# Optimization experiments

Measured on AMD Instinct MI355X. Metric: run time of the kernel, lower is better.

## Reference

```python
import jax, jax.numpy as jnp
import numpy as np

NUM_CLASSES = 81
THRESHOLD = 0.5
NEGPOS_RATIO = 3
VARIANCE = (0.1, 0.2)
B, P, O = 32, 24564, 50


def point_form(pr):
    # center-form (cx,cy,w,h) -> corner-form (x1,y1,x2,y2)
    return jnp.concatenate([pr[:, :2] - pr[:, 2:] / 2, pr[:, :2] + pr[:, 2:] / 2], axis=1)


def jaccard(a, b):
    # a: [O,4] corner-form truths, b: [P,4] corner-form priors -> [O,P]
    lt = jnp.maximum(a[:, None, :2], b[None, :, :2])
    rb = jnp.minimum(a[:, None, 2:], b[None, :, 2:])
    wh = jnp.clip(rb - lt, 0.0)
    inter = wh[..., 0] * wh[..., 1]
    area_a = ((a[:, 2] - a[:, 0]) * (a[:, 3] - a[:, 1]))[:, None]
    area_b = ((b[:, 2] - b[:, 0]) * (b[:, 3] - b[:, 1]))[None, :]
    return inter / (area_a + area_b - inter)


def encode(matched, priors_cf):
    # matched: [P,4] corner-form gt; priors_cf: [P,4] center-form
    g_cxcy = ((matched[:, :2] + matched[:, 2:]) / 2 - priors_cf[:, :2]) / (VARIANCE[0] * priors_cf[:, 2:])
    g_wh = jnp.log((matched[:, 2:] - matched[:, :2]) / priors_cf[:, 2:]) / VARIANCE[1]
    return jnp.concatenate([g_cxcy, g_wh], axis=1)


def match_one(truths, labels, priors_cf, priors_pf):
    ov = jaccard(truths, priors_pf)                       # [O,P]
    best_prior_idx = jnp.argmax(ov, axis=1)               # [O] best prior per truth
    best_truth_overlap = jnp.max(ov, axis=0)              # [P]
    best_truth_idx = jnp.argmax(ov, axis=0)               # [P]
    # ensure every gt matches its best prior
    best_truth_overlap = best_truth_overlap.at[best_prior_idx].set(2.0)
    best_truth_idx = best_truth_idx.at[best_prior_idx].set(jnp.arange(truths.shape[0]))
    matches = truths[best_truth_idx]                      # [P,4]
    conf = labels[best_truth_idx] + 1                     # background = 0
    conf = jnp.where(best_truth_overlap < THRESHOLD, 0, conf)
    loc = encode(matches, priors_cf)
    return loc, conf


def setup_inputs() -> dict:
    key = jax.random.key(0)
    k1, k2, k3, k4, k5, k6, k7 = jax.random.split(key, 7)
    loc_data = jax.random.normal(k1, (B, P, 4), jnp.float32)
    conf_data = jax.random.normal(k2, (B, P, NUM_CLASSES), jnp.float32)
    cxcy = jax.random.uniform(k3, (P, 2), minval=0.05, maxval=0.95)
    wh = jax.random.uniform(k4, (P, 2), minval=0.05, maxval=0.5)
    priors = jnp.concatenate([cxcy, wh], axis=1).astype(jnp.float32)
    gc = jax.random.uniform(k5, (B, O, 2), minval=0.1, maxval=0.9)
    gwh = jax.random.uniform(k6, (B, O, 2), minval=0.05, maxval=0.4)
    boxes = jnp.clip(jnp.concatenate([gc - gwh / 2, gc + gwh / 2], axis=-1), 0.0, 1.0)
    labels = jax.random.randint(k7, (B, O), 0, NUM_CLASSES - 1).astype(jnp.float32)
    targets = jnp.concatenate([boxes, labels[..., None]], axis=-1).astype(jnp.float32)
    return {"loc_data": loc_data, "conf_data": conf_data, "priors": priors, "targets": targets}


def reference(loc_data, conf_data, priors, targets):
    truths = targets[..., :4]                              # [B,O,4]
    labels = targets[..., 4].astype(jnp.int32)             # [B,O]
    priors_pf = point_form(priors)
    loc_t, conf_t = jax.vmap(match_one, in_axes=(0, 0, None, None))(truths, labels, priors, priors_pf)
    pos = conf_t > 0                                       # [B,P]

    # localization smooth-L1 over positives (sum reduction)
    diff = loc_data - loc_t
    sl1 = jnp.where(jnp.abs(diff) < 1.0, 0.5 * diff * diff, jnp.abs(diff) - 0.5)
    loss_l = jnp.sum(sl1 * pos[..., None].astype(sl1.dtype))

    # per-anchor CE loss for hard negative mining
    lse = jax.nn.logsumexp(conf_data, axis=-1)             # [B,P]
    gathered = jnp.take_along_axis(conf_data, conf_t[..., None], axis=-1)[..., 0]
    loss_c_all = lse - gathered                            # [B,P]
    loss_c_mine = jnp.where(pos, 0.0, loss_c_all)
    loss_idx = jnp.argsort(-loss_c_mine, axis=1)
    idx_rank = jnp.argsort(loss_idx, axis=1)
    num_pos = jnp.sum(pos.astype(jnp.int32), axis=1, keepdims=True)  # [B,1]
    num_neg = jnp.minimum(NEGPOS_RATIO * num_pos, P - 1)
    neg = idx_rank < num_neg                               # [B,P]

    sel = jnp.logical_or(pos, neg)
    loss_c = jnp.sum(jnp.where(sel, loss_c_all, 0.0))

    N = jnp.sum(num_pos).astype(loss_l.dtype)
    return loss_l / N, loss_c / N
```

## Files before the change

kernel.cpp:

```cpp
#include <hip/hip_runtime.h>

#define NB 32
#define NP 24564
#define NO 50
#define NC 81
#define THR 0.5f

__device__ __forceinline__ float rl_f(float v, int j) {
  return __uint_as_float((unsigned)__builtin_amdgcn_readlane((int)__float_as_uint(v), j));
}
__device__ __forceinline__ float bp_f(float v, int j4) {
  return __uint_as_float((unsigned)__builtin_amdgcn_ds_bpermute(j4, (int)__float_as_uint(v)));
}


__global__ __launch_bounds__(256) void k0(
    double* __restrict__ acc, int* __restrict__ num_pos,
    float* __restrict__ accLb, float* __restrict__ accCb,
    int* __restrict__ done, unsigned long long* __restrict__ bp) {
  const int tid = threadIdx.x;
  if (tid < 4) acc[tid] = 0.0;
  if (tid < NB) { num_pos[tid] = 0; accLb[tid] = 0.0f; accCb[tid] = 0.0f; }
  if (tid == 4) *done = 0;
  for (int i = tid; i < NB * NO; i += 256) bp[i] = 0ull;
}

#define KA_CHUNK 1024

__global__ __launch_bounds__(256) void kA(
    const float* __restrict__ priors, const float* __restrict__ targets,
    unsigned long long* __restrict__ bp_packed) {
  __shared__ float4 s_pf[KA_CHUNK];
  __shared__ float s_t[NO * 5];
  const int b = blockIdx.y;
  const int tid = threadIdx.x;
  const int base = blockIdx.x * KA_CHUNK;

  for (int i = tid; i < NO * 5; i += 256) s_t[i] = targets[b * NO * 5 + i];

  #pragma unroll
  for (int k = 0; k < KA_CHUNK / 256; ++k) {
    const int p = base + k * 256 + tid;
    float4 pf;
    if (p < NP) {
      const float4 pr = ((const float4*)priors)[p];
      pf = make_float4(pr.x - pr.z * 0.5f, pr.y - pr.w * 0.5f,
                       pr.x + pr.z * 0.5f, pr.y + pr.w * 0.5f);
    } else {
      pf = make_float4(3.0f, 3.0f, 3.0f, 3.0f);
    }
    s_pf[k * 256 + tid] = pf;
  }
  __syncthreads();

  const int wv = tid >> 6;
  const int lane = tid & 63;
  if (lane < NO) {
    const float tx1 = s_t[lane * 5 + 0], ty1 = s_t[lane * 5 + 1];
    const float tx2 = s_t[lane * 5 + 2], ty2 = s_t[lane * 5 + 3];
    const float area_a = (tx2 - tx1) * (ty2 - ty1);
    const int i0 = wv * (KA_CHUNK / 4);
    unsigned long long best = 0ull;
    #pragma unroll 8
    for (int i = 0; i < KA_CHUNK / 4; ++i) {
      const float4 q = s_pf[i0 + i];
      const float ltx = fmaxf(tx1, q.x), lty = fmaxf(ty1, q.y);
      const float rbx = fminf(tx2, q.z), rby = fminf(ty2, q.w);
      const float wx = fmaxf(rbx - ltx, 0.0f), wy = fmaxf(rby - lty, 0.0f);
      const float inter = wx * wy;
      const float ab = (q.z - q.x) * (q.w - q.y);
      const float iou = __fdividef(inter, area_a + ab - inter);
      const unsigned p = (unsigned)(base + i0 + i);
      const unsigned long long pk =
          (((unsigned long long)__float_as_uint(iou)) << 32) |
          (unsigned long long)(0xFFFFFFFFu - p);
      if (pk > best) best = pk;
    }
    atomicMax(&bp_packed[b * NO + lane], best);
  }
}

__global__ __launch_bounds__(256) void kMS(
    const float* __restrict__ loc, const float* __restrict__ conf,
    const float* __restrict__ priors, const float* __restrict__ targets,
    const unsigned* __restrict__ bp32,
    float* __restrict__ mine, int* __restrict__ num_pos,
    float* __restrict__ accLb, float* __restrict__ accCb) {
  __shared__ float s_s[256];
  __shared__ float sLw[4], sCw[4];
  __shared__ int sNw[4];
  const int tid = threadIdx.x;
  const int lane = tid & 63;
  const int b = blockIdx.y;
  const int rowbase = blockIdx.x * 256 + (tid & 192);
  const int p = rowbase + lane;
  const bool valid = (p < NP);
  const int pc = valid ? p : NP - 1;
  const size_t grow = (size_t)b * NP + pc;
  const float* tb = targets + (size_t)b * (NO * 5);

  float ttx1 = 3.f, tty1 = 3.f, ttx2 = 3.f, tty2 = 3.f, tar = 0.f, tlab = 0.f;
  int tpb = -1;
  if (lane < NO) {
    ttx1 = tb[lane * 5 + 0]; tty1 = tb[lane * 5 + 1];
    ttx2 = tb[lane * 5 + 2]; tty2 = tb[lane * 5 + 3];
    tlab = tb[lane * 5 + 4];
    tar = (ttx2 - ttx1) * (tty2 - tty1);
    tpb = (int)(0xFFFFFFFFu - bp32[(b * NO + lane) * 2]);
  }

  const float4 pr = ((const float4*)priors)[pc];
  const float4 ldv = ((const float4*)loc)[grow];
  const float px1 = pr.x - pr.z * 0.5f, py1 = pr.y - pr.w * 0.5f;
  const float px2 = pr.x + pr.z * 0.5f, py2 = pr.y + pr.w * 0.5f;
  const float areab = (px2 - px1) * (py2 - py1);

  float bv = -1.0f;
  int bj = 0;
  #pragma unroll 2
  for (int j = 0; j < NO; ++j) {
    const float x1 = rl_f(ttx1, j), y1 = rl_f(tty1, j);
    const float x2 = rl_f(ttx2, j), y2 = rl_f(tty2, j);
    const float aa = rl_f(tar, j);
    const float wx = fmaxf(fminf(x2, px2) - fmaxf(x1, px1), 0.0f);
    const float wy = fmaxf(fminf(y2, py2) - fmaxf(y1, py1), 0.0f);
    const float inter = wx * wy;
    const float iou = __fdividef(inter, aa + areab - inter);
    if (iou > bv) { bv = iou; bj = j; }
  }

  int ovj = -1;
  unsigned long long M = __ballot((lane < NO) && ((unsigned)(tpb - rowbase) < 64u));
  while (M) {
    const int l = __ffsll((long long)M) - 1;
    M &= M - 1;
    const int r = __builtin_amdgcn_readlane(tpb, l) - rowbase;
    if (lane == r) ovj = l;
  }
  const int jm = (ovj >= 0) ? ovj : bj;
  const bool pos = valid && ((ovj >= 0) || (bv >= THR));
  const int j4 = jm << 2;
  const float lab = bp_f(tlab, j4);
  const float mx1 = bp_f(ttx1, j4), my1 = bp_f(tty1, j4);
  const float mx2 = bp_f(ttx2, j4), my2 = bp_f(tty2, j4);
  const int conft = pos ? ((int)lab + 1) : 0;

  const float gval = conf[grow * NC + conft];

  float sl1 = 0.0f;
  if (pos) {
    const float gcx = __fdividef((mx1 + mx2) * 0.5f - pr.x, 0.1f * pr.z);
    const float gcy = __fdividef((my1 + my2) * 0.5f - pr.y, 0.1f * pr.w);
    const float gw = __logf(__fdividef(mx2 - mx1, pr.z)) * 5.0f;
    const float gh = __logf(__fdividef(my2 - my1, pr.w)) * 5.0f;
    const float d0 = ldv.x - gcx, d1 = ldv.y - gcy;
    const float d2 = ldv.z - gw, d3 = ldv.w - gh;
    #pragma unroll
    for (int q = 0; q < 4; ++q) {
      const float d = (q == 0) ? d0 : (q == 1) ? d1 : (q == 2) ? d2 : d3;
      const float a = fabsf(d);
      sl1 += (a < 1.0f) ? 0.5f * d * d : a - 0.5f;
    }
  }

  const int l16 = lane & 15;
  const int g4 = (lane >> 4) & 3;
  #pragma unroll 2
  for (int ph = 0; ph < 16; ++ph) {
    const int ro = ph * 4 + g4;
    const int rr = rowbase + ro;
    const int rc = (rr < NP) ? rr : NP - 1;
    const float* rowp = conf + ((size_t)b * NP + rc) * NC;
    float s0 = __expf(rowp[l16]);
    float s1 = __expf(rowp[l16 + 16]);
    s0 += __expf(rowp[l16 + 32]);
    s1 += __expf(rowp[l16 + 48]);
    s0 += __expf(rowp[l16 + 64]);
    if (l16 == 0) s1 += __expf(rowp[80]);
    float s = s0 + s1;
    s += __shfl_xor(s, 1, 64);
    s += __shfl_xor(s, 2, 64);
    s += __shfl_xor(s, 4, 64);
    s += __shfl_xor(s, 8, 64);
    if (l16 == 0) s_s[(tid & 192) + ro] = s;
  }
  const float myS = s_s[tid];

  const float lca = __logf(myS) - gval;
  float sumL = 0.0f, sumC = 0.0f;
  int cnt = 0;
  if (valid) {
    mine[grow] = pos ? 0.0f : fmaxf(lca, 0.0f);
    if (pos) { cnt = 1; sumC = lca; sumL = sl1; }
  }

  #pragma unroll
  for (int m = 1; m <= 32; m <<= 1) {
    sumL += __shfl_xor(sumL, m, 64);
    sumC += __shfl_xor(sumC, m, 64);
    cnt  += __shfl_xor(cnt, m, 64);
  }
  const int w = tid >> 6;
  if (lane == 0) { sLw[w] = sumL; sCw[w] = sumC; sNw[w] = cnt; }
  __syncthreads();
  if (tid == 0) {
    const float L = sLw[0] + sLw[1] + sLw[2] + sLw[3];
    const float C = sCw[0] + sCw[1] + sCw[2] + sCw[3];
    const int n = sNw[0] + sNw[1] + sNw[2] + sNw[3];
    if (L != 0.0f) atomicAdd(&accLb[b], L);
    if (C != 0.0f) atomicAdd(&accCb[b], C);
    if (n) atomicAdd(&num_pos[b], n);
  }
}

__global__ __launch_bounds__(512) void kD(
    const float* __restrict__ mine, const int* __restrict__ num_pos,
    double* __restrict__ acc, int* __restrict__ done,
    const float* __restrict__ accLb, const float* __restrict__ accCb,
    float* __restrict__ out) {
  const int b = blockIdx.x;
  const int tid = threadIdx.x;
  const float* vb = mine + (size_t)b * NP;

  unsigned vals[48];
  #pragma unroll
  for (int k = 0; k < 48; ++k) {
    const int i = tid + k * 512;
    vals[k] = (i < NP) ? __float_as_uint(vb[i]) : 0u;
  }

  const int K = min(3 * num_pos[b], NP - 1);

  __shared__ int s_w[2][8];
  unsigned prefix = 0u;
  int remaining = K;

  for (int bit = 30; bit >= 0; --bit) {
    const unsigned want = (prefix >> bit) | 1u;
    int cnt = 0;
    #pragma unroll
    for (int k = 0; k < 48; ++k) cnt += ((vals[k] >> bit) == want) ? 1 : 0;
    #pragma unroll
    for (int m = 32; m >= 1; m >>= 1) cnt += __shfl_xor(cnt, m, 64);
    const int buf = bit & 1;
    if ((tid & 63) == 0) s_w[buf][tid >> 6] = cnt;
    __syncthreads();
    int total = 0;
    #pragma unroll
    for (int w = 0; w < 8; ++w) total += s_w[buf][w];
    if (total >= remaining) prefix |= (1u << bit);
    else remaining -= total;
  }

  if (K > 0) {
    const float t = __uint_as_float(prefix);
    double sg = 0.0;
    int cg = 0;
    #pragma unroll
    for (int k = 0; k < 48; ++k) {
      const float f = __uint_as_float(vals[k]);
      if (f > t) { sg += (double)f; cg++; }
    }
    #pragma unroll
    for (int m = 32; m >= 1; m >>= 1) {
      sg += __shfl_xor(sg, m, 64);
      cg += __shfl_xor(cg, m, 64);
    }
    __shared__ double s_sd[8];
    __shared__ int s_sc[8];
    const int wid = tid >> 6;
    if ((tid & 63) == 0) { s_sd[wid] = sg; s_sc[wid] = cg; }
    __syncthreads();
    if (tid == 0) {
      double S = 0.0;
      int C = 0;
      for (int w = 0; w < 8; ++w) { S += s_sd[w]; C += s_sc[w]; }
      S += (double)(K - C) * (double)t;
      atomicAdd(&acc[2], S);
    }
  }

  __shared__ int s_last;
  __syncthreads();
  if (tid == 0) {
    __threadfence();
    s_last = (atomicAdd(done, 1) == NB - 1) ? 1 : 0;
  }
  __syncthreads();
  if (s_last && tid < 64) {
    int n = 0;
    float L = 0.0f, C = 0.0f;
    if (tid < NB) { n = num_pos[tid]; L = accLb[tid]; C = accCb[tid]; }
    #pragma unroll
    for (int m = 32; m >= 1; m >>= 1) {
      n += __shfl_xor(n, m, 64);
      L += __shfl_xor(L, m, 64);
      C += __shfl_xor(C, m, 64);
    }
    if (tid == 0) {
      const double S = atomicAdd(&acc[2], 0.0);
      const double Nf = (double)n;
      out[0] = (float)((double)L / Nf);
      out[1] = (float)(((double)C + S) / Nf);
    }
  }
}

extern "C" void kernel_launch(void* const* d_in, const int* in_sizes, int n_in,
                              void* d_out, int out_size, void* d_ws, size_t ws_size,
                              hipStream_t stream) {
  const float* loc     = (const float*)d_in[0];
  const float* conf    = (const float*)d_in[1];
  const float* priors  = (const float*)d_in[2];
  const float* targets = (const float*)d_in[3];
  float* out = (float*)d_out;

  char* ws = (char*)d_ws;
  double* acc   = (double*)ws;
  int* num_pos  = (int*)(ws + 32);
  float* accLb  = (float*)(ws + 160);
  float* accCb  = (float*)(ws + 288);
  int* done     = (int*)(ws + 416);
  unsigned long long* bp = (unsigned long long*)(ws + 424);
  const size_t hdr = 13224;
  float* mine  = (float*)(ws + hdr);

  k0<<<1, 256, 0, stream>>>(acc, num_pos, accLb, accCb, done, bp);

  dim3 gA((NP + KA_CHUNK - 1) / KA_CHUNK, NB);
  kA<<<gA, 256, 0, stream>>>(priors, targets, bp);

  dim3 gM((NP + 255) / 256, NB);
  kMS<<<gM, 256, 0, stream>>>(loc, conf, priors, targets, (const unsigned*)bp,
                              mine, num_pos, accLb, accCb);

  kD<<<NB, 512, 0, stream>>>(mine, num_pos, acc, done, accLb, accCb, out);
}
```

Measured before the change: 159.2 us.

## Drop init kernel and atomics via per-chunk best-prior partials; vectorize conf row loads

```diff
diff --git a/kernel.cpp b/kernel.cpp
--- a/kernel.cpp
+++ b/kernel.cpp
@@ -5,6 +5,8 @@
 #define NO 50
 #define NC 81
 #define THR 0.5f
+#define KA_CHUNK 1024
+#define NCH 24
 
 __device__ __forceinline__ float rl_f(float v, int j) {
   return __uint_as_float((unsigned)__builtin_amdgcn_readlane((int)__float_as_uint(v), j));
@@ -14,27 +16,26 @@
 }
 
 
-__global__ __launch_bounds__(256) void k0(
+__global__ __launch_bounds__(256) void kA(
+    const float* __restrict__ priors, const float* __restrict__ targets,
+    unsigned long long* __restrict__ bpc,
     double* __restrict__ acc, int* __restrict__ num_pos,
     float* __restrict__ accLb, float* __restrict__ accCb,
-    int* __restrict__ done, unsigned long long* __restrict__ bp) {
-  const int tid = threadIdx.x;
-  if (tid < 4) acc[tid] = 0.0;
-  if (tid < NB) { num_pos[tid] = 0; accLb[tid] = 0.0f; accCb[tid] = 0.0f; }
-  if (tid == 4) *done = 0;
-  for (int i = tid; i < NB * NO; i += 256) bp[i] = 0ull;
-}
-
-#define KA_CHUNK 1024
-
-__global__ __launch_bounds__(256) void kA(
-    const float* __restrict__ priors, const float* __restrict__ targets,
-    unsigned long long* __restrict__ bp_packed) {
+    int* __restrict__ done) {
   __shared__ float4 s_pf[KA_CHUNK];
   __shared__ float s_t[NO * 5];
+  __shared__ unsigned long long s_bp[256];
   const int b = blockIdx.y;
   const int tid = threadIdx.x;
   const int base = blockIdx.x * KA_CHUNK;
+
+  if (blockIdx.x == 0 && b == 0) {
+    if (tid < 4) acc[tid] = 0.0;
+    else if (tid >= 32 && tid < 64) num_pos[tid - 32] = 0;
+    else if (tid >= 64 && tid < 96) accLb[tid - 64] = 0.0f;
+    else if (tid >= 96 && tid < 128) accCb[tid - 96] = 0.0f;
+    else if (tid == 128) *done = 0;
+  }
 
   for (int i = tid; i < NO * 5; i += 256) s_t[i] = targets[b * NO * 5 + i];
 
@@ -55,18 +56,17 @@
 
   const int wv = tid >> 6;
   const int lane = tid & 63;
+  unsigned long long best = 0ull;
   if (lane < NO) {
     const float tx1 = s_t[lane * 5 + 0], ty1 = s_t[lane * 5 + 1];
     const float tx2 = s_t[lane * 5 + 2], ty2 = s_t[lane * 5 + 3];
     const float area_a = (tx2 - tx1) * (ty2 - ty1);
-    const int i0 = wv * (KA_CHUNK / 4);
-    unsigned long long best = 0ull;
+    const int i0 = wv * 256;
     #pragma unroll 8
-    for (int i = 0; i < KA_CHUNK / 4; ++i) {
+    for (int i = 0; i < 256; ++i) {
       const float4 q = s_pf[i0 + i];
-      const float ltx = fmaxf(tx1, q.x), lty = fmaxf(ty1, q.y);
-      const float rbx = fminf(tx2, q.z), rby = fminf(ty2, q.w);
-      const float wx = fmaxf(rbx - ltx, 0.0f), wy = fmaxf(rby - lty, 0.0f);
+      const float wx = fmaxf(fminf(q.z, tx2) - fmaxf(q.x, tx1), 0.0f);
+      const float wy = fmaxf(fminf(q.w, ty2) - fmaxf(q.y, ty1), 0.0f);
       const float inter = wx * wy;
       const float ab = (q.z - q.x) * (q.w - q.y);
       const float iou = __fdividef(inter, area_a + ab - inter);
@@ -76,17 +76,26 @@
           (unsigned long long)(0xFFFFFFFFu - p);
       if (pk > best) best = pk;
     }
-    atomicMax(&bp_packed[b * NO + lane], best);
+  }
+  s_bp[tid] = best;
+  __syncthreads();
+  if (tid < NO) {
+    unsigned long long m = s_bp[tid];
+    unsigned long long v = s_bp[64 + tid];  if (v > m) m = v;
+    v = s_bp[128 + tid];                    if (v > m) m = v;
+    v = s_bp[192 + tid];                    if (v > m) m = v;
+    bpc[(size_t)(b * NO + tid) * NCH + blockIdx.x] = m;
   }
 }
 
 __global__ __launch_bounds__(256) void kMS(
     const float* __restrict__ loc, const float* __restrict__ conf,
     const float* __restrict__ priors, const float* __restrict__ targets,
-    const unsigned* __restrict__ bp32,
+    const unsigned long long* __restrict__ bpc,
     float* __restrict__ mine, int* __restrict__ num_pos,
     float* __restrict__ accLb, float* __restrict__ accCb) {
   __shared__ float s_s[256];
+  __shared__ int s_tpb[NO];
   __shared__ float sLw[4], sCw[4];
   __shared__ int sNw[4];
   const int tid = threadIdx.x;
@@ -99,21 +108,31 @@
   const size_t grow = (size_t)b * NP + pc;
   const float* tb = targets + (size_t)b * (NO * 5);
 
+  if (tid < NO) {
+    const unsigned long long* sl = bpc + (size_t)(b * NO + tid) * NCH;
+    unsigned long long m = 0ull;
+    #pragma unroll
+    for (int c = 0; c < NCH; ++c) {
+      const unsigned long long v = sl[c];
+      if (v > m) m = v;
+    }
+    s_tpb[tid] = (int)(0xFFFFFFFFu - (unsigned)(m & 0xFFFFFFFFull));
+  }
+
   float ttx1 = 3.f, tty1 = 3.f, ttx2 = 3.f, tty2 = 3.f, tar = 0.f, tlab = 0.f;
-  int tpb = -1;
   if (lane < NO) {
     ttx1 = tb[lane * 5 + 0]; tty1 = tb[lane * 5 + 1];
     ttx2 = tb[lane * 5 + 2]; tty2 = tb[lane * 5 + 3];
     tlab = tb[lane * 5 + 4];
     tar = (ttx2 - ttx1) * (tty2 - tty1);
-    tpb = (int)(0xFFFFFFFFu - bp32[(b * NO + lane) * 2]);
-  }
-
+  }
   const float4 pr = ((const float4*)priors)[pc];
   const float4 ldv = ((const float4*)loc)[grow];
   const float px1 = pr.x - pr.z * 0.5f, py1 = pr.y - pr.w * 0.5f;
   const float px2 = pr.x + pr.z * 0.5f, py2 = pr.y + pr.w * 0.5f;
   const float areab = (px2 - px1) * (py2 - py1);
+  __syncthreads();
+  const int tpb = (lane < NO) ? s_tpb[lane] : -1;
 
   float bv = -1.0f;
   int bj = 0;
@@ -145,8 +164,6 @@
   const float mx2 = bp_f(ttx2, j4), my2 = bp_f(tty2, j4);
   const int conft = pos ? ((int)lab + 1) : 0;
 
-  const float gval = conf[grow * NC + conft];
-
   float sl1 = 0.0f;
   if (pos) {
     const float gcx = __fdividef((mx1 + mx2) * 0.5f - pr.x, 0.1f * pr.z);
@@ -165,19 +182,18 @@
 
   const int l16 = lane & 15;
   const int g4 = (lane >> 4) & 3;
+  const int c0 = (4 - g4) & 3;
   #pragma unroll 2
   for (int ph = 0; ph < 16; ++ph) {
     const int ro = ph * 4 + g4;
     const int rr = rowbase + ro;
     const int rc = (rr < NP) ? rr : NP - 1;
     const float* rowp = conf + ((size_t)b * NP + rc) * NC;
-    float s0 = __expf(rowp[l16]);
-    float s1 = __expf(rowp[l16 + 16]);
-    s0 += __expf(rowp[l16 + 32]);
-    s1 += __expf(rowp[l16 + 48]);
-    s0 += __expf(rowp[l16 + 64]);
-    if (l16 == 0) s1 += __expf(rowp[80]);
-    float s = s0 + s1;
+    const float4 v = *(const float4*)(rowp + c0 + 4 * l16);
+    float s = __expf(v.x) + __expf(v.y) + __expf(v.z) + __expf(v.w);
+    const int tc = (l16 < c0) ? l16 : (c0 + 64 + (l16 - c0));
+    s += __expf(rowp[tc]);
+    if (l16 == 0) s += __expf(rowp[80]);
     s += __shfl_xor(s, 1, 64);
     s += __shfl_xor(s, 2, 64);
     s += __shfl_xor(s, 4, 64);
@@ -186,7 +202,9 @@
   }
   const float myS = s_s[tid];
 
+  const float gval = conf[grow * NC + conft];
   const float lca = __logf(myS) - gval;
+
   float sumL = 0.0f, sumC = 0.0f;
   int cnt = 0;
   if (valid) {
@@ -321,17 +339,16 @@
   float* accLb  = (float*)(ws + 160);
   float* accCb  = (float*)(ws + 288);
   int* done     = (int*)(ws + 416);
-  unsigned long long* bp = (unsigned long long*)(ws + 424);
-  const size_t hdr = 13224;
+  unsigned long long* bpc = (unsigned long long*)(ws + 424);
+  const size_t hdr = 424 + (size_t)NB * NO * NCH * 8;
   float* mine  = (float*)(ws + hdr);
 
-  k0<<<1, 256, 0, stream>>>(acc, num_pos, accLb, accCb, done, bp);
-
-  dim3 gA((NP + KA_CHUNK - 1) / KA_CHUNK, NB);
-  kA<<<gA, 256, 0, stream>>>(priors, targets, bp);
+  dim3 gA(NCH, NB);
+  kA<<<gA, 256, 0, stream>>>(priors, targets, bpc,
+                             acc, num_pos, accLb, accCb, done);
 
   dim3 gM((NP + 255) / 256, NB);
-  kMS<<<gM, 256, 0, stream>>>(loc, conf, priors, targets, (const unsigned*)bp,
+  kMS<<<gM, 256, 0, stream>>>(loc, conf, priors, targets, bpc,
                               mine, num_pos, accLb, accCb);
 
   kD<<<NB, 512, 0, stream>>>(mine, num_pos, acc, done, accLb, accCb, out);
```

New measurement: 154.0 us. 1.03x faster.
